# Performance work log

Measured on AMD Instinct MI355X. Metric: run time of the kernel, lower is better.

## Reference

```python
import jax, jax.numpy as jnp
import numpy as np

R = 3.82843
FREQ = 1.0
ITERATIONS = 2

def activation_fn(x):
    # cosine squashing into [0,1], then two logistic-map iterations
    x = jnp.cos(x * FREQ) * 0.5 + 0.5
    for _ in range(ITERATIONS):
        x = R * x * (1.0 - x)
    return x

def setup_inputs() -> dict:
    key = jax.random.key(0)
    ks = jax.random.split(key, 9)
    N = 2097152
    x = jax.random.normal(ks[0], (N, 2), dtype=jnp.float32)
    def init_linear(kw, kb, fan_in, fan_out):
        # torch.nn.Linear default init: U(-1/sqrt(fan_in), 1/sqrt(fan_in))
        bound = 1.0 / np.sqrt(fan_in)
        W = jax.random.uniform(kw, (fan_out, fan_in), minval=-bound, maxval=bound, dtype=jnp.float32)
        b = jax.random.uniform(kb, (fan_out,), minval=-bound, maxval=bound, dtype=jnp.float32)
        return W, b
    W1, b1 = init_linear(ks[1], ks[2], 2, 64)
    W2, b2 = init_linear(ks[3], ks[4], 64, 64)
    W3, b3 = init_linear(ks[5], ks[6], 64, 64)
    W4, b4 = init_linear(ks[7], ks[8], 64, 1)
    return {"x": x, "W1": W1, "b1": b1, "W2": W2, "b2": b2,
            "W3": W3, "b3": b3, "W4": W4, "b4": b4}

def reference(x, W1, b1, W2, b2, W3, b3, W4, b4):
    h = activation_fn(x @ W1.T + b1)   # [N, 64]
    h = activation_fn(h @ W2.T + b2)   # [N, 64]
    h = activation_fn(h @ W3.T + b3)   # [N, 64]
    out = activation_fn(h @ W4.T + b4) # [N, 1]
    return out
```

## Files before the change

### kernel.cpp

```cpp
#include <hip/hip_runtime.h>

typedef _Float16 half8  __attribute__((ext_vector_type(8)));
typedef _Float16 half4v __attribute__((ext_vector_type(4)));
typedef _Float16 half2v __attribute__((ext_vector_type(2)));
typedef float    floatx4 __attribute__((ext_vector_type(4)));
typedef float    float2v __attribute__((ext_vector_type(2)));

static constexpr float INVPI = 0.3183098861837907f;
static constexpr float RLOG  = 3.82843f;

static constexpr double RD = (double)RLOG;
static constexpr double AD = RD*RD/4.0 - RD*RD*RD/16.0;
static constexpr double BD = -RD*RD/4.0 + RD*RD*RD/8.0;
static constexpr double DD = -RD*RD*RD/16.0;
static constexpr float ACT_E = (float)(AD + BD/2.0 + DD/4.0);
static constexpr float ACT_F = (float)((BD + DD)/2.0);
static constexpr float ACT_G = (float)(DD/4.0);

__device__ __forceinline__ float act_rev(float a2) {
    float c = __builtin_amdgcn_cosf(a2);
    float t = __builtin_fmaf(ACT_G, c, ACT_F);
    return __builtin_fmaf(c, t, ACT_E);
}

__device__ __forceinline__ half8 act8(floatx4 a, floatx4 b) {
    const half2v Gh = {(_Float16)ACT_G, (_Float16)ACT_G};
    const half2v Fh = {(_Float16)ACT_F, (_Float16)ACT_F};
    const half2v Eh = {(_Float16)ACT_E, (_Float16)ACT_E};
    half2v c0 = __builtin_bit_cast(half2v, __builtin_amdgcn_cvt_pkrtz(
                    __builtin_amdgcn_cosf(a[0]), __builtin_amdgcn_cosf(a[1])));
    half2v c1 = __builtin_bit_cast(half2v, __builtin_amdgcn_cvt_pkrtz(
                    __builtin_amdgcn_cosf(a[2]), __builtin_amdgcn_cosf(a[3])));
    half2v c2 = __builtin_bit_cast(half2v, __builtin_amdgcn_cvt_pkrtz(
                    __builtin_amdgcn_cosf(b[0]), __builtin_amdgcn_cosf(b[1])));
    half2v c3 = __builtin_bit_cast(half2v, __builtin_amdgcn_cvt_pkrtz(
                    __builtin_amdgcn_cosf(b[2]), __builtin_amdgcn_cosf(b[3])));
    half2v t0 = __builtin_elementwise_fma(c0, Gh, Fh);
    half2v t1 = __builtin_elementwise_fma(c1, Gh, Fh);
    half2v t2 = __builtin_elementwise_fma(c2, Gh, Fh);
    half2v t3 = __builtin_elementwise_fma(c3, Gh, Fh);
    half2v h0 = __builtin_elementwise_fma(c0, t0, Eh);
    half2v h1 = __builtin_elementwise_fma(c1, t1, Eh);
    half2v h2 = __builtin_elementwise_fma(c2, t2, Eh);
    half2v h3 = __builtin_elementwise_fma(c3, t3, Eh);
    half4v lo = __builtin_shufflevector(h0, h1, 0, 1, 2, 3);
    half4v hi = __builtin_shufflevector(h2, h3, 0, 1, 2, 3);
    return __builtin_shufflevector(lo, hi, 0, 1, 2, 3, 4, 5, 6, 7);
}

struct SMem {
    half8   w2[8][64];
    half8   w3[8][64];
    floatx4 b2[4][64];
    floatx4 b3[4][64];
};

__global__ __launch_bounds__(512, 8) void mlp_fused(
    const float* __restrict__ x,
    const float* __restrict__ W1, const float* __restrict__ b1,
    const float* __restrict__ W2, const float* __restrict__ b2,
    const float* __restrict__ W3, const float* __restrict__ b3,
    const float* __restrict__ W4, const float* __restrict__ b4,
    float* __restrict__ out, int N)
{
    __shared__ SMem sm;
    const int lane = threadIdx.x & 63;
    const int wib  = threadIdx.x >> 6;
    const int m    = lane & 15;
    const int q    = lane >> 4;
    const float s  = INVPI;
    const floatx4 zero4 = {0.0f, 0.0f, 0.0f, 0.0f};

    half8 w1f[4];
    #pragma unroll
    for (int t = 0; t < 4; ++t) {
        half8 v = {};
        if (q == 0) {
            const int n = 16 * t + m;
            float w0 = W1[2*n] * s, w1 = W1[2*n+1] * s, bb = b1[n] * s;
            _Float16 w0h = (_Float16)w0; float w0l = w0 - (float)w0h;
            _Float16 w1h = (_Float16)w1; float w1l = w1 - (float)w1h;
            _Float16 bh  = (_Float16)bb; float bl  = bb - (float)bh;
            v[0] = w0h; v[1] = w0h; v[2] = (_Float16)w0l;
            v[3] = w1h; v[4] = w1h; v[5] = (_Float16)w1l;
            v[6] = bh;  v[7] = (_Float16)bl;
        }
        w1f[t] = v;
    }
    half8 w4f[2] = {half8{}, half8{}};
    if (m == 0) {
        #pragma unroll
        for (int c = 0; c < 2; ++c)
            #pragma unroll
            for (int j = 0; j < 8; ++j) {
                int nu = (j < 4) ? (16 * c + 4 * q + j) : (16 * (c + 2) + 4 * q + j - 4);
                w4f[c][j] = (_Float16)(W4[nu] * s);
            }
    }
    floatx4 a4init = zero4;
    if (q == 0) a4init[0] = b4[0] * s;

    if (wib == 0) {
        #pragma unroll
        for (int t = 0; t < 4; ++t) {
            const float* r2 = W2 + (16 * t + m) * 64;
            #pragma unroll
            for (int c = 0; c < 2; ++c) {
                floatx4 lo2 = *(const floatx4*)(r2 + 16 * c + 4 * q);
                floatx4 hi2 = *(const floatx4*)(r2 + 16 * (c + 2) + 4 * q);
                half8 v2;
                #pragma unroll
                for (int j = 0; j < 4; ++j) {
                    v2[j]     = (_Float16)(lo2[j] * s);
                    v2[4 + j] = (_Float16)(hi2[j] * s);
                }
                sm.w2[t * 2 + c][lane] = v2;
            }
        }
    } else if (wib == 1) {
        #pragma unroll
        for (int t = 0; t < 4; ++t) {
            const float* r3 = W3 + (16 * t + m) * 64;
            #pragma unroll
            for (int c = 0; c < 2; ++c) {
                floatx4 lo3 = *(const floatx4*)(r3 + 16 * c + 4 * q);
                floatx4 hi3 = *(const floatx4*)(r3 + 16 * (c + 2) + 4 * q);
                half8 v3;
                #pragma unroll
                for (int j = 0; j < 4; ++j) {
                    v3[j]     = (_Float16)(lo3[j] * s);
                    v3[4 + j] = (_Float16)(hi3[j] * s);
                }
                sm.w3[t * 2 + c][lane] = v3;
            }
        }
    } else if (wib == 2) {
        #pragma unroll
        for (int t = 0; t < 4; ++t) {
            sm.b2[t][lane] = *(const floatx4*)(b2 + 16 * t + 4 * q) * s;
            sm.b3[t][lane] = *(const floatx4*)(b3 + 16 * t + 4 * q) * s;
        }
    }
    __syncthreads();

    const int ntiles = N >> 4;
    const int nwaves = (gridDim.x * blockDim.x) >> 6;
    const int gwave  = (int)(blockIdx.x * blockDim.x + threadIdx.x) >> 6;
    const float2* __restrict__ x2 = (const float2*)x;

    int tile = gwave;
    float2 xv = x2[(tile << 4) + m];
    while (tile < ntiles) {
        const int nt = tile + nwaves;
        float2 xnext;
        if (nt < ntiles) xnext = x2[(nt << 4) + m];

        half8 xa = {};
        if (q == 0) {
            _Float16 xh = (_Float16)xv.x; float xl = xv.x - (float)xh;
            _Float16 yh = (_Float16)xv.y; float yl = xv.y - (float)yh;
            xa[0] = xh; xa[1] = (_Float16)xl; xa[2] = xh;
            xa[3] = yh; xa[4] = (_Float16)yl; xa[5] = yh;
            xa[6] = (_Float16)1.0f; xa[7] = (_Float16)1.0f;
        }

        floatx4 a0 = __builtin_amdgcn_mfma_f32_16x16x32_f16(w1f[0], xa, zero4, 0, 0, 0);
        floatx4 a1 = __builtin_amdgcn_mfma_f32_16x16x32_f16(w1f[1], xa, zero4, 0, 0, 0);
        floatx4 a2 = __builtin_amdgcn_mfma_f32_16x16x32_f16(w1f[2], xa, zero4, 0, 0, 0);
        floatx4 a3 = __builtin_amdgcn_mfma_f32_16x16x32_f16(w1f[3], xa, zero4, 0, 0, 0);
        half8 B0 = act8(a0, a2);
        half8 B1 = act8(a1, a3);

        int z2 = 0; asm volatile("" : "+v"(z2));
        const int l2i = lane + z2;
        a0 = __builtin_amdgcn_mfma_f32_16x16x32_f16(sm.w2[0][l2i], B0, sm.b2[0][l2i], 0, 0, 0);
        a1 = __builtin_amdgcn_mfma_f32_16x16x32_f16(sm.w2[2][l2i], B0, sm.b2[1][l2i], 0, 0, 0);
        a2 = __builtin_amdgcn_mfma_f32_16x16x32_f16(sm.w2[4][l2i], B0, sm.b2[2][l2i], 0, 0, 0);
        a3 = __builtin_amdgcn_mfma_f32_16x16x32_f16(sm.w2[6][l2i], B0, sm.b2[3][l2i], 0, 0, 0);
        a0 = __builtin_amdgcn_mfma_f32_16x16x32_f16(sm.w2[1][l2i], B1, a0, 0, 0, 0);
        a1 = __builtin_amdgcn_mfma_f32_16x16x32_f16(sm.w2[3][l2i], B1, a1, 0, 0, 0);
        a2 = __builtin_amdgcn_mfma_f32_16x16x32_f16(sm.w2[5][l2i], B1, a2, 0, 0, 0);
        a3 = __builtin_amdgcn_mfma_f32_16x16x32_f16(sm.w2[7][l2i], B1, a3, 0, 0, 0);
        half8 C0 = act8(a0, a2);
        half8 C1 = act8(a1, a3);

        int z3 = 0; asm volatile("" : "+v"(z3));
        const int l3i = lane + z3;
        a0 = __builtin_amdgcn_mfma_f32_16x16x32_f16(sm.w3[0][l3i], C0, sm.b3[0][l3i], 0, 0, 0);
        a1 = __builtin_amdgcn_mfma_f32_16x16x32_f16(sm.w3[2][l3i], C0, sm.b3[1][l3i], 0, 0, 0);
        a2 = __builtin_amdgcn_mfma_f32_16x16x32_f16(sm.w3[4][l3i], C0, sm.b3[2][l3i], 0, 0, 0);
        a3 = __builtin_amdgcn_mfma_f32_16x16x32_f16(sm.w3[6][l3i], C0, sm.b3[3][l3i], 0, 0, 0);
        a0 = __builtin_amdgcn_mfma_f32_16x16x32_f16(sm.w3[1][l3i], C1, a0, 0, 0, 0);
        a1 = __builtin_amdgcn_mfma_f32_16x16x32_f16(sm.w3[3][l3i], C1, a1, 0, 0, 0);
        a2 = __builtin_amdgcn_mfma_f32_16x16x32_f16(sm.w3[5][l3i], C1, a2, 0, 0, 0);
        a3 = __builtin_amdgcn_mfma_f32_16x16x32_f16(sm.w3[7][l3i], C1, a3, 0, 0, 0);
        half8 D0 = act8(a0, a2);
        half8 D1 = act8(a1, a3);

        floatx4 a4 = __builtin_amdgcn_mfma_f32_16x16x32_f16(w4f[0], D0, a4init, 0, 0, 0);
        a4 = __builtin_amdgcn_mfma_f32_16x16x32_f16(w4f[1], D1, a4, 0, 0, 0);
        if (q == 0)
            out[(tile << 4) + m] = act_rev(a4[0]);

        xv = xnext;
        tile = nt;
    }
}

extern "C" void kernel_launch(void* const* d_in, const int* in_sizes, int n_in,
                              void* d_out, int out_size, void* d_ws, size_t ws_size,
                              hipStream_t stream) {
    const float* x  = (const float*)d_in[0];
    const float* W1 = (const float*)d_in[1];
    const float* b1 = (const float*)d_in[2];
    const float* W2 = (const float*)d_in[3];
    const float* b2 = (const float*)d_in[4];
    const float* W3 = (const float*)d_in[5];
    const float* b3 = (const float*)d_in[6];
    const float* W4 = (const float*)d_in[7];
    const float* b4 = (const float*)d_in[8];
    float* out = (float*)d_out;
    const int N = out_size;

    mlp_fused<<<dim3(2048), dim3(512), 0, stream>>>(x, W1, b1, W2, b2, W3, b3, W4, b4, out, N);
}
```

Before: 144.9 us.

## Process two tiles per wave iteration and switch to 256-thread blocks

Each wave now handles two independent 16-row tiles per loop iteration, interleaving their MFMA chains and activations to expose more instruction-level parallelism and reuse the LDS weight reads. Input prefetch is extended to two tiles ahead, with clamped indices. Launch shape changes from 2048x512 with launch bounds (512,8) to 4096x256 with (256,4), which relaxes the register limit to hold the doubled live state. The cost is higher register pressure, possibly lower occupancy, and a guarded store for the second tile.

```diff
diff --git a/kernel.cpp b/kernel.cpp
--- a/kernel.cpp
+++ b/kernel.cpp
@@ -55,7 +55,7 @@
     floatx4 b3[4][64];
 };
 
-__global__ __launch_bounds__(512, 8) void mlp_fused(
+__global__ __launch_bounds__(256, 4) void mlp_fused(
     const float* __restrict__ x,
     const float* __restrict__ W1, const float* __restrict__ b1,
     const float* __restrict__ W2, const float* __restrict__ b2,
@@ -147,62 +147,105 @@
     const int nwaves = (gridDim.x * blockDim.x) >> 6;
     const int gwave  = (int)(blockIdx.x * blockDim.x + threadIdx.x) >> 6;
     const float2* __restrict__ x2 = (const float2*)x;
+    const int tmax = ntiles - 1;
 
     int tile = gwave;
-    float2 xv = x2[(tile << 4) + m];
+    float2 xv0 = x2[(min(tile, tmax) << 4) + m];
+    float2 xv1 = x2[(min(tile + nwaves, tmax) << 4) + m];
     while (tile < ntiles) {
-        const int nt = tile + nwaves;
-        float2 xnext;
-        if (nt < ntiles) xnext = x2[(nt << 4) + m];
-
-        half8 xa = {};
+        const int t1 = tile + nwaves;
+        const int nt = tile + 2 * nwaves;
+        float2 xn0, xn1;
+        if (nt < ntiles) {
+            xn0 = x2[(nt << 4) + m];
+            xn1 = x2[(min(nt + nwaves, tmax) << 4) + m];
+        }
+
+        half8 xa0 = {}, xa1 = {};
         if (q == 0) {
-            _Float16 xh = (_Float16)xv.x; float xl = xv.x - (float)xh;
-            _Float16 yh = (_Float16)xv.y; float yl = xv.y - (float)yh;
-            xa[0] = xh; xa[1] = (_Float16)xl; xa[2] = xh;
-            xa[3] = yh; xa[4] = (_Float16)yl; xa[5] = yh;
-            xa[6] = (_Float16)1.0f; xa[7] = (_Float16)1.0f;
-        }
-
-        floatx4 a0 = __builtin_amdgcn_mfma_f32_16x16x32_f16(w1f[0], xa, zero4, 0, 0, 0);
-        floatx4 a1 = __builtin_amdgcn_mfma_f32_16x16x32_f16(w1f[1], xa, zero4, 0, 0, 0);
-        floatx4 a2 = __builtin_amdgcn_mfma_f32_16x16x32_f16(w1f[2], xa, zero4, 0, 0, 0);
-        floatx4 a3 = __builtin_amdgcn_mfma_f32_16x16x32_f16(w1f[3], xa, zero4, 0, 0, 0);
-        half8 B0 = act8(a0, a2);
-        half8 B1 = act8(a1, a3);
+            _Float16 xh = (_Float16)xv0.x; float xl = xv0.x - (float)xh;
+            _Float16 yh = (_Float16)xv0.y; float yl = xv0.y - (float)yh;
+            xa0[0] = xh; xa0[1] = (_Float16)xl; xa0[2] = xh;
+            xa0[3] = yh; xa0[4] = (_Float16)yl; xa0[5] = yh;
+            xa0[6] = (_Float16)1.0f; xa0[7] = (_Float16)1.0f;
+            _Float16 xh1 = (_Float16)xv1.x; float xl1 = xv1.x - (float)xh1;
+            _Float16 yh1 = (_Float16)xv1.y; float yl1 = xv1.y - (float)yh1;
+            xa1[0] = xh1; xa1[1] = (_Float16)xl1; xa1[2] = xh1;
+            xa1[3] = yh1; xa1[4] = (_Float16)yl1; xa1[5] = yh1;
+            xa1[6] = (_Float16)1.0f; xa1[7] = (_Float16)1.0f;
+        }
+
+        floatx4 a0 = __builtin_amdgcn_mfma_f32_16x16x32_f16(w1f[0], xa0, zero4, 0, 0, 0);
+        floatx4 e0 = __builtin_amdgcn_mfma_f32_16x16x32_f16(w1f[0], xa1, zero4, 0, 0, 0);
+        floatx4 a1 = __builtin_amdgcn_mfma_f32_16x16x32_f16(w1f[1], xa0, zero4, 0, 0, 0);
+        floatx4 e1 = __builtin_amdgcn_mfma_f32_16x16x32_f16(w1f[1], xa1, zero4, 0, 0, 0);
+        floatx4 a2 = __builtin_amdgcn_mfma_f32_16x16x32_f16(w1f[2], xa0, zero4, 0, 0, 0);
+        floatx4 e2 = __builtin_amdgcn_mfma_f32_16x16x32_f16(w1f[2], xa1, zero4, 0, 0, 0);
+        floatx4 a3 = __builtin_amdgcn_mfma_f32_16x16x32_f16(w1f[3], xa0, zero4, 0, 0, 0);
+        floatx4 e3 = __builtin_amdgcn_mfma_f32_16x16x32_f16(w1f[3], xa1, zero4, 0, 0, 0);
+        half8 B0  = act8(a0, a2);
+        half8 B1  = act8(a1, a3);
+        half8 B0b = act8(e0, e2);
+        half8 B1b = act8(e1, e3);
 
         int z2 = 0; asm volatile("" : "+v"(z2));
         const int l2i = lane + z2;
         a0 = __builtin_amdgcn_mfma_f32_16x16x32_f16(sm.w2[0][l2i], B0, sm.b2[0][l2i], 0, 0, 0);
+        e0 = __builtin_amdgcn_mfma_f32_16x16x32_f16(sm.w2[0][l2i], B0b, sm.b2[0][l2i], 0, 0, 0);
         a1 = __builtin_amdgcn_mfma_f32_16x16x32_f16(sm.w2[2][l2i], B0, sm.b2[1][l2i], 0, 0, 0);
+        e1 = __builtin_amdgcn_mfma_f32_16x16x32_f16(sm.w2[2][l2i], B0b, sm.b2[1][l2i], 0, 0, 0);
         a2 = __builtin_amdgcn_mfma_f32_16x16x32_f16(sm.w2[4][l2i], B0, sm.b2[2][l2i], 0, 0, 0);
+        e2 = __builtin_amdgcn_mfma_f32_16x16x32_f16(sm.w2[4][l2i], B0b, sm.b2[2][l2i], 0, 0, 0);
         a3 = __builtin_amdgcn_mfma_f32_16x16x32_f16(sm.w2[6][l2i], B0, sm.b2[3][l2i], 0, 0, 0);
+        e3 = __builtin_amdgcn_mfma_f32_16x16x32_f16(sm.w2[6][l2i], B0b, sm.b2[3][l2i], 0, 0, 0);
         a0 = __builtin_amdgcn_mfma_f32_16x16x32_f16(sm.w2[1][l2i], B1, a0, 0, 0, 0);
+        e0 = __builtin_amdgcn_mfma_f32_16x16x32_f16(sm.w2[1][l2i], B1b, e0, 0, 0, 0);
         a1 = __builtin_amdgcn_mfma_f32_16x16x32_f16(sm.w2[3][l2i], B1, a1, 0, 0, 0);
+        e1 = __builtin_amdgcn_mfma_f32_16x16x32_f16(sm.w2[3][l2i], B1b, e1, 0, 0, 0);
         a2 = __builtin_amdgcn_mfma_f32_16x16x32_f16(sm.w2[5][l2i], B1, a2, 0, 0, 0);
+        e2 = __builtin_amdgcn_mfma_f32_16x16x32_f16(sm.w2[5][l2i], B1b, e2, 0, 0, 0);
         a3 = __builtin_amdgcn_mfma_f32_16x16x32_f16(sm.w2[7][l2i], B1, a3, 0, 0, 0);
-        half8 C0 = act8(a0, a2);
-        half8 C1 = act8(a1, a3);
+        e3 = __builtin_amdgcn_mfma_f32_16x16x32_f16(sm.w2[7][l2i], B1b, e3, 0, 0, 0);
+        half8 C0  = act8(a0, a2);
+        half8 C1  = act8(a1, a3);
+        half8 C0b = act8(e0, e2);
+        half8 C1b = act8(e1, e3);
 
         int z3 = 0; asm volatile("" : "+v"(z3));
         const int l3i = lane + z3;
         a0 = __builtin_amdgcn_mfma_f32_16x16x32_f16(sm.w3[0][l3i], C0, sm.b3[0][l3i], 0, 0, 0);
+        e0 = __builtin_amdgcn_mfma_f32_16x16x32_f16(sm.w3[0][l3i], C0b, sm.b3[0][l3i], 0, 0, 0);
         a1 = __builtin_amdgcn_mfma_f32_16x16x32_f16(sm.w3[2][l3i], C0, sm.b3[1][l3i], 0, 0, 0);
+        e1 = __builtin_amdgcn_mfma_f32_16x16x32_f16(sm.w3[2][l3i], C0b, sm.b3[1][l3i], 0, 0, 0);
         a2 = __builtin_amdgcn_mfma_f32_16x16x32_f16(sm.w3[4][l3i], C0, sm.b3[2][l3i], 0, 0, 0);
+        e2 = __builtin_amdgcn_mfma_f32_16x16x32_f16(sm.w3[4][l3i], C0b, sm.b3[2][l3i], 0, 0, 0);
         a3 = __builtin_amdgcn_mfma_f32_16x16x32_f16(sm.w3[6][l3i], C0, sm.b3[3][l3i], 0, 0, 0);
+        e3 = __builtin_amdgcn_mfma_f32_16x16x32_f16(sm.w3[6][l3i], C0b, sm.b3[3][l3i], 0, 0, 0);
         a0 = __builtin_amdgcn_mfma_f32_16x16x32_f16(sm.w3[1][l3i], C1, a0, 0, 0, 0);
+        e0 = __builtin_amdgcn_mfma_f32_16x16x32_f16(sm.w3[1][l3i], C1b, e0, 0, 0, 0);
         a1 = __builtin_amdgcn_mfma_f32_16x16x32_f16(sm.w3[3][l3i], C1, a1, 0, 0, 0);
+        e1 = __builtin_amdgcn_mfma_f32_16x16x32_f16(sm.w3[3][l3i], C1b, e1, 0, 0, 0);
         a2 = __builtin_amdgcn_mfma_f32_16x16x32_f16(sm.w3[5][l3i], C1, a2, 0, 0, 0);
+        e2 = __builtin_amdgcn_mfma_f32_16x16x32_f16(sm.w3[5][l3i], C1b, e2, 0, 0, 0);
         a3 = __builtin_amdgcn_mfma_f32_16x16x32_f16(sm.w3[7][l3i], C1, a3, 0, 0, 0);
-        half8 D0 = act8(a0, a2);
-        half8 D1 = act8(a1, a3);
+        e3 = __builtin_amdgcn_mfma_f32_16x16x32_f16(sm.w3[7][l3i], C1b, e3, 0, 0, 0);
+        half8 D0  = act8(a0, a2);
+        half8 D1  = act8(a1, a3);
+        half8 D0b = act8(e0, e2);
+        half8 D1b = act8(e1, e3);
 
         floatx4 a4 = __builtin_amdgcn_mfma_f32_16x16x32_f16(w4f[0], D0, a4init, 0, 0, 0);
         a4 = __builtin_amdgcn_mfma_f32_16x16x32_f16(w4f[1], D1, a4, 0, 0, 0);
-        if (q == 0)
+        floatx4 a4b = __builtin_amdgcn_mfma_f32_16x16x32_f16(w4f[0], D0b, a4init, 0, 0, 0);
+        a4b = __builtin_amdgcn_mfma_f32_16x16x32_f16(w4f[1], D1b, a4b, 0, 0, 0);
+        if (q == 0) {
             out[(tile << 4) + m] = act_rev(a4[0]);
-
-        xv = xnext;
+            if (t1 < ntiles)
+                out[(t1 << 4) + m] = act_rev(a4b[0]);
+        }
+
+        xv0 = xn0;
+        xv1 = xn1;
         tile = nt;
     }
 }
@@ -222,5 +265,5 @@
     float* out = (float*)d_out;
     const int N = out_size;
 
-    mlp_fused<<<dim3(2048), dim3(512), 0, stream>>>(x, W1, b1, W2, b2, W3, b3, W4, b4, out, N);
-}
+    mlp_fused<<<dim3(4096), dim3(256), 0, stream>>>(x, W1, b1, W2, b2, W3, b3, W4, b4, out, N);
+}
```

Result: no change. 147.3 us (+1.6%).
